# Performance work log

Measured on AMD Instinct MI355X. Metric: run time of the kernel, lower is better.

Reference implementation:

```python
import jax, jax.numpy as jnp
import numpy as np

B, S, A, MSG, C = 524288, 64, 16, 32, 4
CH = 9 + S  # children_states feature dim = 73
EPS = 1e-12  # F.normalize clamp_min eps


def _l2norm(v):
    n = jnp.sqrt(jnp.sum(v * v, axis=-1, keepdims=True))
    return v / jnp.maximum(n, EPS)


def setup_inputs() -> dict:
    key = jax.random.key(0)
    ks = jax.random.split(key, 12)
    def lin(kw, kb, out_d, in_d):
        bound = 1.0 / np.sqrt(in_d)
        W = jax.random.uniform(kw, (out_d, in_d), minval=-bound, maxval=bound, dtype=jnp.float32)
        b = jax.random.uniform(kb, (out_d,), minval=-bound, maxval=bound, dtype=jnp.float32)
        return W, b
    W1, b1 = lin(ks[0], ks[1], 64, S + A)
    W2, b2 = lin(ks[2], ks[3], 64, 64 + MSG)
    W3, b3 = lin(ks[4], ks[5], MSG, 64)
    Wa, ba = lin(ks[6], ks[7], MSG, CH)
    return {
        "x": jax.random.normal(ks[8], (B, S), dtype=jnp.float32),
        "u": jax.random.normal(ks[9], (B, A), dtype=jnp.float32),
        "children_states": jax.random.normal(ks[10], (B, C, CH), dtype=jnp.float32),
        "m": jax.random.normal(ks[11], (B, C * MSG), dtype=jnp.float32),
        "W1": W1, "b1": b1, "W2": W2, "b2": b2, "W3": W3, "b3": b3,
        "Wa": Wa, "ba": ba,
    }


def reference(x, u, children_states, m, W1, b1, W2, b2, W3, b3, Wa, ba):
    # fc1 on cat(x, u), then L2 normalize
    xu = jnp.concatenate([x, u], axis=-1) @ W1.T + b1          # [B, 64]
    xu = _l2norm(xu)
    # attention over children (softmax along child axis, dim=-2)
    att = jax.nn.softmax(children_states @ Wa.T + ba, axis=-2)  # [B, C, MSG]
    mm = m.reshape(*children_states.shape[:-1], -1)             # [B, C, MSG]
    magg = jnp.sum(mm * att, axis=-2)                           # [B, MSG]
    # fused MLP tail
    xum = jnp.tanh(jnp.concatenate([xu, magg], axis=-1))        # [B, 64+MSG]
    xum = jnp.tanh(xum @ W2.T + b2)                             # [B, 64]
    xum = xum @ W3.T + b3                                       # [B, MSG]
    return _l2norm(xum)
```

## Files before the change

### kernel.cpp

```cpp
#include <hip/hip_runtime.h>
#include <cstddef>

typedef __fp16 f16x8 __attribute__((ext_vector_type(8)));
typedef float f32x4 __attribute__((ext_vector_type(4)));
typedef unsigned int uint32;
typedef unsigned short ushort;

constexpr int S = 64, MSG = 32, CH = 73;

constexpr int FC1_OFF = 0;
constexpr int ATT_OFF = 12 * 512;
constexpr int FC2_OFF = 18 * 512;
constexpr int FC3_OFF = 30 * 512;
constexpr int WS_ELEMS = 34 * 512;

__global__ void prep_pack(const float* __restrict__ W1, const float* __restrict__ b1,
                          const float* __restrict__ Wa, const float* __restrict__ ba,
                          const float* __restrict__ W2, const float* __restrict__ W3,
                          ushort* __restrict__ wsf) {
  int idx = blockIdx.x * 256 + threadIdx.x;
  if (idx >= WS_ELEMS) return;
  int tile = idx >> 9;
  int lane = (idx >> 3) & 63;
  int e = idx & 7;
  int jloc = lane & 15;
  int kloc = ((lane >> 4) << 3) + e;
  float v = 0.f;
  if (tile < 12) {
    int t = tile >> 2, f = tile & 3;
    int j = f * 16 + jloc, k = t * 32 + kloc;
    v = (k < 80) ? W1[j * 80 + k] : (k == 80 ? b1[j] : 0.f);
  } else if (tile < 18) {
    int q = tile - 12, t = q >> 1, f = q & 1;
    int j = f * 16 + jloc, k = t * 32 + kloc;
    v = (k < 73) ? Wa[j * 73 + k] : (k == 73 ? ba[j] : 0.f);
  } else if (tile < 30) {
    int q = tile - 18, t = q >> 2, f = q & 3;
    int j = f * 16 + jloc, k = t * 32 + kloc;
    v = W2[j * 96 + k];
  } else {
    int q = tile - 30, t = q >> 1, f = q & 1;
    int j = f * 16 + jloc, k = t * 32 + kloc;
    v = W3[j * 64 + k];
  }
  union { __fp16 h; ushort s; } cv;
  cv.h = (__fp16)v;
  wsf[idx] = cv.s;
}

__device__ __forceinline__ f32x4 mf(f16x8 a, f16x8 b, f32x4 c) {
  return __builtin_amdgcn_mfma_f32_16x16x32_f16(a, b, c, 0, 0, 0);
}
__device__ __forceinline__ uint32 pku(float a, float b) {
  auto r = __builtin_amdgcn_cvt_pkrtz(a, b);
  union { decltype(r) f; uint32 u; } v; v.f = r; return v.u;
}
__device__ __forceinline__ f16x8 packA(const float* f) {
  union { uint32 u[4]; f16x8 h; } r;
  r.u[0] = pku(f[0], f[1]); r.u[1] = pku(f[2], f[3]);
  r.u[2] = pku(f[4], f[5]); r.u[3] = pku(f[6], f[7]);
  return r.h;
}
__device__ __forceinline__ f16x8 packA2(float4 a, float4 b) {
  union { uint32 u[4]; f16x8 h; } r;
  r.u[0] = pku(a.x, a.y); r.u[1] = pku(a.z, a.w);
  r.u[2] = pku(b.x, b.y); r.u[3] = pku(b.z, b.w);
  return r.h;
}
__device__ __forceinline__ float fast_tanh(float v) {
  v = fminf(15.f, fmaxf(-15.f, v));
  float t = __expf(2.f * v);
  return (t - 1.f) * __builtin_amdgcn_rcpf(t + 1.f);
}

constexpr int HT_LD = 104;
constexpr int H2_LD = 72;
constexpr int HBUF_B = 3328;
constexpr int UNION_OFF = 13312;
constexpr int UNION_B = 4672;
constexpr int SMEM_B = 32000;

__launch_bounds__(256)
__global__ void critic_mfma_kernel(
    const float* __restrict__ x, const float* __restrict__ u,
    const float* __restrict__ cs, const float* __restrict__ m,
    const float* __restrict__ b2, const float* __restrict__ b3,
    const ushort* __restrict__ wsf, float* __restrict__ out, int n) {
  __shared__ __attribute__((aligned(16))) unsigned char smem[SMEM_B];

  const int wave = threadIdx.x >> 6;
  const int lane = threadIdx.x & 63;
  const int lm = lane & 15;
  const int lq = lane >> 4;
  const int r0 = (blockIdx.x * 4 + wave) * 16;
  if (r0 >= n) return;

  __fp16* __restrict__ ht = reinterpret_cast<__fp16*>(smem + wave * HBUF_B);
  float* __restrict__ csw = reinterpret_cast<float*>(smem + UNION_OFF + wave * UNION_B);
  __fp16* __restrict__ h2t = reinterpret_cast<__fp16*>(smem + UNION_OFF + wave * UNION_B);

  const float4* __restrict__ xrow4 =
      reinterpret_cast<const float4*>(x + (size_t)(r0 + lm) * S);
  float4 xva = xrow4[2 * lq], xvb = xrow4[2 * lq + 1];
  float4 xvc = xrow4[8 + 2 * lq], xvd = xrow4[9 + 2 * lq];
  const int uq = (lq < 2) ? lq : 0;
  const float4* __restrict__ urow4 =
      reinterpret_cast<const float4*>(u + (size_t)(r0 + lm) * 16);
  float4 uva = urow4[2 * uq], uvb = urow4[2 * uq + 1];

  auto ldB = [&](int off_tile) -> f16x8 {
    return *reinterpret_cast<const f16x8*>(wsf + off_tile + lane * 8);
  };

  f16x8 wa[6];
#pragma unroll
  for (int i = 0; i < 6; ++i) wa[i] = ldB(ATT_OFF + i * 512);

  float4 csr0, csr1, csr2, csr3, csr4;
  {
    const float4* __restrict__ src =
        reinterpret_cast<const float4*>(cs + (size_t)(r0 * 4) * CH);
    csr0 = src[lane];       csr1 = src[64 + lane];
    csr2 = src[128 + lane]; csr3 = src[192 + lane];
    if (lane < 36) csr4 = src[256 + lane];
  }

#pragma unroll
  for (int g = 0; g < 4; ++g) {
    {
      float4* __restrict__ dst = reinterpret_cast<float4*>(csw);
      dst[lane] = csr0;       dst[64 + lane] = csr1;
      dst[128 + lane] = csr2; dst[192 + lane] = csr3;
      if (lane < 36) dst[256 + lane] = csr4;
    }
    float mr[8];
    {
      const float* __restrict__ mrow = m + (size_t)(r0 + 4 * g + lq) * 128;
#pragma unroll
      for (int c = 0; c < 4; ++c) {
        mr[c * 2 + 0] = mrow[c * 32 + lm];
        mr[c * 2 + 1] = mrow[c * 32 + lm + 16];
      }
    }
    if (g < 3) {
      const float4* __restrict__ src =
          reinterpret_cast<const float4*>(cs + (size_t)(r0 * 4 + 16 * (g + 1)) * CH);
      csr0 = src[lane];       csr1 = src[64 + lane];
      csr2 = src[128 + lane]; csr3 = src[192 + lane];
      if (lane < 36) csr4 = src[256 + lane];
    }
    const float* __restrict__ crow = csw + lm * CH;
    f32x4 zac[2] = {{0.f, 0.f, 0.f, 0.f}, {0.f, 0.f, 0.f, 0.f}};
#pragma unroll
    for (int t = 0; t < 3; ++t) {
      float f[8];
      const int kbase = t * 32 + lq * 8;
#pragma unroll
      for (int e = 0; e < 8; ++e) {
        int k = kbase + e;
        f[e] = (k < 73) ? crow[k] : (k == 73 ? 1.f : 0.f);
      }
      f16x8 af = packA(f);
      zac[0] = mf(af, wa[t * 2 + 0], zac[0]);
      zac[1] = mf(af, wa[t * 2 + 1], zac[1]);
    }
#pragma unroll
    for (int f = 0; f < 2; ++f) {
      const int j = lm + 16 * f;
      float e0 = __expf(zac[f][0]);
      float e1 = __expf(zac[f][1]);
      float e2 = __expf(zac[f][2]);
      float e3 = __expf(zac[f][3]);
      float den = (e0 + e1) + (e2 + e3);
      float num = fmaf(mr[0 * 2 + f], e0,
                  fmaf(mr[1 * 2 + f], e1,
                  fmaf(mr[2 * 2 + f], e2, mr[3 * 2 + f] * e3)));
      float mg = num * __builtin_amdgcn_rcpf(den);
      ht[(4 * g + lq) * HT_LD + 64 + j] = (__fp16)fast_tanh(mg);
    }
  }

  f32x4 hac[4] = {{0.f,0.f,0.f,0.f},{0.f,0.f,0.f,0.f},{0.f,0.f,0.f,0.f},{0.f,0.f,0.f,0.f}};
  {
    f16x8 a0 = packA2(xva, xvb);
    f16x8 a1 = packA2(xvc, xvd);
#pragma unroll
    for (int fi = 0; fi < 4; ++fi) hac[fi] = mf(a0, ldB(FC1_OFF + fi * 512), hac[fi]);
#pragma unroll
    for (int fi = 0; fi < 4; ++fi) hac[fi] = mf(a1, ldB(FC1_OFF + (4 + fi) * 512), hac[fi]);
    float f[8];
    float uf[8] = {uva.x, uva.y, uva.z, uva.w, uvb.x, uvb.y, uvb.z, uvb.w};
#pragma unroll
    for (int e = 0; e < 8; ++e) {
      int k = 64 + lq * 8 + e;
      f[e] = (k < 80) ? ((lq < 2) ? uf[e] : 0.f) : (k == 80 ? 1.f : 0.f);
    }
    f16x8 a2f = packA(f);
#pragma unroll
    for (int fi = 0; fi < 4; ++fi) hac[fi] = mf(a2f, ldB(FC1_OFF + (8 + fi) * 512), hac[fi]);
  }
  {
    float rn[4];
#pragma unroll
    for (int reg = 0; reg < 4; ++reg) {
      float s = hac[0][reg] * hac[0][reg];
      s = fmaf(hac[1][reg], hac[1][reg], s);
      s = fmaf(hac[2][reg], hac[2][reg], s);
      s = fmaf(hac[3][reg], hac[3][reg], s);
      s += __shfl_xor(s, 1);
      s += __shfl_xor(s, 2);
      s += __shfl_xor(s, 4);
      s += __shfl_xor(s, 8);
      rn[reg] = __builtin_amdgcn_rcpf(fmaxf(sqrtf(s), 1e-12f));
    }
#pragma unroll
    for (int fi = 0; fi < 4; ++fi)
#pragma unroll
      for (int reg = 0; reg < 4; ++reg)
        ht[(4 * lq + reg) * HT_LD + lm + 16 * fi] =
            (__fp16)fast_tanh(hac[fi][reg] * rn[reg]);
  }

  {
    f32x4 ac2[4] = {{0.f,0.f,0.f,0.f},{0.f,0.f,0.f,0.f},{0.f,0.f,0.f,0.f},{0.f,0.f,0.f,0.f}};
    f16x8 a2[3];
#pragma unroll
    for (int t = 0; t < 3; ++t)
      a2[t] = *reinterpret_cast<const f16x8*>(ht + lm * HT_LD + t * 32 + lq * 8);
#pragma unroll
    for (int t = 0; t < 3; ++t)
#pragma unroll
      for (int fi = 0; fi < 4; ++fi)
        ac2[fi] = mf(a2[t], ldB(FC2_OFF + (t * 4 + fi) * 512), ac2[fi]);
#pragma unroll
    for (int fi = 0; fi < 4; ++fi) {
      float bv = b2[lm + 16 * fi];
#pragma unroll
      for (int reg = 0; reg < 4; ++reg)
        h2t[(4 * lq + reg) * H2_LD + lm + 16 * fi] =
            (__fp16)fast_tanh(ac2[fi][reg] + bv);
    }
  }

  {
    f32x4 o[2] = {{0.f,0.f,0.f,0.f},{0.f,0.f,0.f,0.f}};
    f16x8 a3[2];
#pragma unroll
    for (int t = 0; t < 2; ++t)
      a3[t] = *reinterpret_cast<const f16x8*>(h2t + lm * H2_LD + t * 32 + lq * 8);
#pragma unroll
    for (int t = 0; t < 2; ++t)
#pragma unroll
      for (int fi = 0; fi < 2; ++fi)
        o[fi] = mf(a3[t], ldB(FC3_OFF + (t * 2 + fi) * 512), o[fi]);
#pragma unroll
    for (int fi = 0; fi < 2; ++fi) {
      float bv = b3[lm + 16 * fi];
#pragma unroll
      for (int reg = 0; reg < 4; ++reg) o[fi][reg] += bv;
    }
    float rn2[4];
#pragma unroll
    for (int reg = 0; reg < 4; ++reg) {
      float s = fmaf(o[0][reg], o[0][reg], o[1][reg] * o[1][reg]);
      s += __shfl_xor(s, 1);
      s += __shfl_xor(s, 2);
      s += __shfl_xor(s, 4);
      s += __shfl_xor(s, 8);
      rn2[reg] = __builtin_amdgcn_rcpf(fmaxf(sqrtf(s), 1e-12f));
    }
#pragma unroll
    for (int fi = 0; fi < 2; ++fi)
#pragma unroll
      for (int reg = 0; reg < 4; ++reg)
        out[(size_t)(r0 + 4 * lq + reg) * MSG + lm + 16 * fi] =
            o[fi][reg] * rn2[reg];
  }
}

extern "C" void kernel_launch(void* const* d_in, const int* in_sizes, int n_in,
                              void* d_out, int out_size, void* d_ws, size_t ws_size,
                              hipStream_t stream) {
  const float* x  = (const float*)d_in[0];
  const float* u  = (const float*)d_in[1];
  const float* cs = (const float*)d_in[2];
  const float* m  = (const float*)d_in[3];
  const float* W1 = (const float*)d_in[4];
  const float* b1 = (const float*)d_in[5];
  const float* W2 = (const float*)d_in[6];
  const float* b2 = (const float*)d_in[7];
  const float* W3 = (const float*)d_in[8];
  const float* b3 = (const float*)d_in[9];
  const float* Wa = (const float*)d_in[10];
  const float* ba = (const float*)d_in[11];
  float* out = (float*)d_out;
  ushort* wsf = (ushort*)d_ws;

  const int n = in_sizes[0] / S;

  hipLaunchKernelGGL(prep_pack, dim3((WS_ELEMS + 255) / 256), dim3(256), 0, stream,
                     W1, b1, Wa, ba, W2, W3, wsf);

  const int blocks = (n + 63) / 64;
  hipLaunchKernelGGL(critic_mfma_kernel, dim3(blocks), dim3(256), 0, stream,
                     x, u, cs, m, b2, b3, wsf, out, n);
}
```

Baseline: 223.8 us.

## Process two tiles per wave and prefetch next tile's inputs across iterations

```diff
diff --git a/kernel.cpp b/kernel.cpp
--- a/kernel.cpp
+++ b/kernel.cpp
@@ -92,22 +92,16 @@
   const int lane = threadIdx.x & 63;
   const int lm = lane & 15;
   const int lq = lane >> 4;
-  const int r0 = (blockIdx.x * 4 + wave) * 16;
-  if (r0 >= n) return;
+
+  const int tiles = n >> 4;
+  const int wslots = gridDim.x * 4;
+  const int tbase = blockIdx.x * 4 + wave;
+  if (tbase >= tiles) return;
 
   __fp16* __restrict__ ht = reinterpret_cast<__fp16*>(smem + wave * HBUF_B);
   float* __restrict__ csw = reinterpret_cast<float*>(smem + UNION_OFF + wave * UNION_B);
   __fp16* __restrict__ h2t = reinterpret_cast<__fp16*>(smem + UNION_OFF + wave * UNION_B);
 
-  const float4* __restrict__ xrow4 =
-      reinterpret_cast<const float4*>(x + (size_t)(r0 + lm) * S);
-  float4 xva = xrow4[2 * lq], xvb = xrow4[2 * lq + 1];
-  float4 xvc = xrow4[8 + 2 * lq], xvd = xrow4[9 + 2 * lq];
-  const int uq = (lq < 2) ? lq : 0;
-  const float4* __restrict__ urow4 =
-      reinterpret_cast<const float4*>(u + (size_t)(r0 + lm) * 16);
-  float4 uva = urow4[2 * uq], uvb = urow4[2 * uq + 1];
-
   auto ldB = [&](int off_tile) -> f16x8 {
     return *reinterpret_cast<const f16x8*>(wsf + off_tile + lane * 8);
   };
@@ -117,164 +111,184 @@
   for (int i = 0; i < 6; ++i) wa[i] = ldB(ATT_OFF + i * 512);
 
   float4 csr0, csr1, csr2, csr3, csr4;
-  {
+  float4 xva, xvb, xvc, xvd, uva, uvb;
+
+  auto issue_cs = [&](int r0, int g) {
     const float4* __restrict__ src =
-        reinterpret_cast<const float4*>(cs + (size_t)(r0 * 4) * CH);
+        reinterpret_cast<const float4*>(cs + (size_t)(r0 * 4 + 16 * g) * CH);
     csr0 = src[lane];       csr1 = src[64 + lane];
     csr2 = src[128 + lane]; csr3 = src[192 + lane];
     if (lane < 36) csr4 = src[256 + lane];
-  }
-
-#pragma unroll
-  for (int g = 0; g < 4; ++g) {
+  };
+  auto issue_xu = [&](int r0) {
+    const float4* __restrict__ xrow4 =
+        reinterpret_cast<const float4*>(x + (size_t)(r0 + lm) * S);
+    xva = xrow4[2 * lq]; xvb = xrow4[2 * lq + 1];
+    xvc = xrow4[8 + 2 * lq]; xvd = xrow4[9 + 2 * lq];
+    const int uq = (lq < 2) ? lq : 0;
+    const float4* __restrict__ urow4 =
+        reinterpret_cast<const float4*>(u + (size_t)(r0 + lm) * 16);
+    uva = urow4[2 * uq]; uvb = urow4[2 * uq + 1];
+  };
+
+  issue_cs(tbase << 4, 0);
+  issue_xu(tbase << 4);
+
+  for (int t = 0; t < 2; ++t) {
+    const int tile = tbase + t * wslots;
+    if (tile >= tiles) break;
+    const int r0 = tile << 4;
+    const int ntile = tile + wslots;
+    const bool pre_next = (t == 0) && (ntile < tiles);
+
+#pragma unroll
+    for (int g = 0; g < 4; ++g) {
+      {
+        float4* __restrict__ dst = reinterpret_cast<float4*>(csw);
+        dst[lane] = csr0;       dst[64 + lane] = csr1;
+        dst[128 + lane] = csr2; dst[192 + lane] = csr3;
+        if (lane < 36) dst[256 + lane] = csr4;
+      }
+      float mr[8];
+      {
+        const float* __restrict__ mrow = m + (size_t)(r0 + 4 * g + lq) * 128;
+#pragma unroll
+        for (int c = 0; c < 4; ++c) {
+          mr[c * 2 + 0] = mrow[c * 32 + lm];
+          mr[c * 2 + 1] = mrow[c * 32 + lm + 16];
+        }
+      }
+      if (g < 3) issue_cs(r0, g + 1);
+      else if (pre_next) issue_cs(ntile << 4, 0);
+
+      const float* __restrict__ crow = csw + lm * CH;
+      f32x4 zac[2] = {{0.f, 0.f, 0.f, 0.f}, {0.f, 0.f, 0.f, 0.f}};
+#pragma unroll
+      for (int tt = 0; tt < 3; ++tt) {
+        float f[8];
+        const int kbase = tt * 32 + lq * 8;
+#pragma unroll
+        for (int e = 0; e < 8; ++e) {
+          int k = kbase + e;
+          f[e] = (k < 73) ? crow[k] : (k == 73 ? 1.f : 0.f);
+        }
+        f16x8 af = packA(f);
+        zac[0] = mf(af, wa[tt * 2 + 0], zac[0]);
+        zac[1] = mf(af, wa[tt * 2 + 1], zac[1]);
+      }
+#pragma unroll
+      for (int f = 0; f < 2; ++f) {
+        const int j = lm + 16 * f;
+        float e0 = __expf(zac[f][0]);
+        float e1 = __expf(zac[f][1]);
+        float e2 = __expf(zac[f][2]);
+        float e3 = __expf(zac[f][3]);
+        float den = (e0 + e1) + (e2 + e3);
+        float num = fmaf(mr[0 * 2 + f], e0,
+                    fmaf(mr[1 * 2 + f], e1,
+                    fmaf(mr[2 * 2 + f], e2, mr[3 * 2 + f] * e3)));
+        float mg = num * __builtin_amdgcn_rcpf(den);
+        ht[(4 * g + lq) * HT_LD + 64 + j] = (__fp16)fast_tanh(mg);
+      }
+    }
+
+    f32x4 hac[4] = {{0.f,0.f,0.f,0.f},{0.f,0.f,0.f,0.f},{0.f,0.f,0.f,0.f},{0.f,0.f,0.f,0.f}};
     {
-      float4* __restrict__ dst = reinterpret_cast<float4*>(csw);
-      dst[lane] = csr0;       dst[64 + lane] = csr1;
-      dst[128 + lane] = csr2; dst[192 + lane] = csr3;
-      if (lane < 36) dst[256 + lane] = csr4;
-    }
-    float mr[8];
+      f16x8 a0 = packA2(xva, xvb);
+      f16x8 a1 = packA2(xvc, xvd);
+      float f[8];
+      float uf[8] = {uva.x, uva.y, uva.z, uva.w, uvb.x, uvb.y, uvb.z, uvb.w};
+#pragma unroll
+      for (int e = 0; e < 8; ++e) {
+        int k = 64 + lq * 8 + e;
+        f[e] = (k < 80) ? ((lq < 2) ? uf[e] : 0.f) : (k == 80 ? 1.f : 0.f);
+      }
+      f16x8 a2f = packA(f);
+      if (pre_next) issue_xu(ntile << 4);
+#pragma unroll
+      for (int fi = 0; fi < 4; ++fi) hac[fi] = mf(a0, ldB(FC1_OFF + fi * 512), hac[fi]);
+#pragma unroll
+      for (int fi = 0; fi < 4; ++fi) hac[fi] = mf(a1, ldB(FC1_OFF + (4 + fi) * 512), hac[fi]);
+#pragma unroll
+      for (int fi = 0; fi < 4; ++fi) hac[fi] = mf(a2f, ldB(FC1_OFF + (8 + fi) * 512), hac[fi]);
+    }
     {
-      const float* __restrict__ mrow = m + (size_t)(r0 + 4 * g + lq) * 128;
-#pragma unroll
-      for (int c = 0; c < 4; ++c) {
-        mr[c * 2 + 0] = mrow[c * 32 + lm];
-        mr[c * 2 + 1] = mrow[c * 32 + lm + 16];
-      }
-    }
-    if (g < 3) {
-      const float4* __restrict__ src =
-          reinterpret_cast<const float4*>(cs + (size_t)(r0 * 4 + 16 * (g + 1)) * CH);
-      csr0 = src[lane];       csr1 = src[64 + lane];
-      csr2 = src[128 + lane]; csr3 = src[192 + lane];
-      if (lane < 36) csr4 = src[256 + lane];
-    }
-    const float* __restrict__ crow = csw + lm * CH;
-    f32x4 zac[2] = {{0.f, 0.f, 0.f, 0.f}, {0.f, 0.f, 0.f, 0.f}};
-#pragma unroll
-    for (int t = 0; t < 3; ++t) {
-      float f[8];
-      const int kbase = t * 32 + lq * 8;
-#pragma unroll
-      for (int e = 0; e < 8; ++e) {
-        int k = kbase + e;
-        f[e] = (k < 73) ? crow[k] : (k == 73 ? 1.f : 0.f);
-      }
-      f16x8 af = packA(f);
-      zac[0] = mf(af, wa[t * 2 + 0], zac[0]);
-      zac[1] = mf(af, wa[t * 2 + 1], zac[1]);
-    }
-#pragma unroll
-    for (int f = 0; f < 2; ++f) {
-      const int j = lm + 16 * f;
-      float e0 = __expf(zac[f][0]);
-      float e1 = __expf(zac[f][1]);
-      float e2 = __expf(zac[f][2]);
-      float e3 = __expf(zac[f][3]);
-      float den = (e0 + e1) + (e2 + e3);
-      float num = fmaf(mr[0 * 2 + f], e0,
-                  fmaf(mr[1 * 2 + f], e1,
-                  fmaf(mr[2 * 2 + f], e2, mr[3 * 2 + f] * e3)));
-      float mg = num * __builtin_amdgcn_rcpf(den);
-      ht[(4 * g + lq) * HT_LD + 64 + j] = (__fp16)fast_tanh(mg);
-    }
-  }
-
-  f32x4 hac[4] = {{0.f,0.f,0.f,0.f},{0.f,0.f,0.f,0.f},{0.f,0.f,0.f,0.f},{0.f,0.f,0.f,0.f}};
-  {
-    f16x8 a0 = packA2(xva, xvb);
-    f16x8 a1 = packA2(xvc, xvd);
-#pragma unroll
-    for (int fi = 0; fi < 4; ++fi) hac[fi] = mf(a0, ldB(FC1_OFF + fi * 512), hac[fi]);
-#pragma unroll
-    for (int fi = 0; fi < 4; ++fi) hac[fi] = mf(a1, ldB(FC1_OFF + (4 + fi) * 512), hac[fi]);
-    float f[8];
-    float uf[8] = {uva.x, uva.y, uva.z, uva.w, uvb.x, uvb.y, uvb.z, uvb.w};
-#pragma unroll
-    for (int e = 0; e < 8; ++e) {
-      int k = 64 + lq * 8 + e;
-      f[e] = (k < 80) ? ((lq < 2) ? uf[e] : 0.f) : (k == 80 ? 1.f : 0.f);
-    }
-    f16x8 a2f = packA(f);
-#pragma unroll
-    for (int fi = 0; fi < 4; ++fi) hac[fi] = mf(a2f, ldB(FC1_OFF + (8 + fi) * 512), hac[fi]);
-  }
-  {
-    float rn[4];
-#pragma unroll
-    for (int reg = 0; reg < 4; ++reg) {
-      float s = hac[0][reg] * hac[0][reg];
-      s = fmaf(hac[1][reg], hac[1][reg], s);
-      s = fmaf(hac[2][reg], hac[2][reg], s);
-      s = fmaf(hac[3][reg], hac[3][reg], s);
-      s += __shfl_xor(s, 1);
-      s += __shfl_xor(s, 2);
-      s += __shfl_xor(s, 4);
-      s += __shfl_xor(s, 8);
-      rn[reg] = __builtin_amdgcn_rcpf(fmaxf(sqrtf(s), 1e-12f));
-    }
-#pragma unroll
-    for (int fi = 0; fi < 4; ++fi)
-#pragma unroll
-      for (int reg = 0; reg < 4; ++reg)
-        ht[(4 * lq + reg) * HT_LD + lm + 16 * fi] =
-            (__fp16)fast_tanh(hac[fi][reg] * rn[reg]);
-  }
-
-  {
-    f32x4 ac2[4] = {{0.f,0.f,0.f,0.f},{0.f,0.f,0.f,0.f},{0.f,0.f,0.f,0.f},{0.f,0.f,0.f,0.f}};
-    f16x8 a2[3];
-#pragma unroll
-    for (int t = 0; t < 3; ++t)
-      a2[t] = *reinterpret_cast<const f16x8*>(ht + lm * HT_LD + t * 32 + lq * 8);
-#pragma unroll
-    for (int t = 0; t < 3; ++t)
+      float rn[4];
+#pragma unroll
+      for (int reg = 0; reg < 4; ++reg) {
+        float s = hac[0][reg] * hac[0][reg];
+        s = fmaf(hac[1][reg], hac[1][reg], s);
+        s = fmaf(hac[2][reg], hac[2][reg], s);
+        s = fmaf(hac[3][reg], hac[3][reg], s);
+        s += __shfl_xor(s, 1);
+        s += __shfl_xor(s, 2);
+        s += __shfl_xor(s, 4);
+        s += __shfl_xor(s, 8);
+        rn[reg] = __builtin_amdgcn_rcpf(fmaxf(sqrtf(s), 1e-12f));
+      }
 #pragma unroll
       for (int fi = 0; fi < 4; ++fi)
-        ac2[fi] = mf(a2[t], ldB(FC2_OFF + (t * 4 + fi) * 512), ac2[fi]);
-#pragma unroll
-    for (int fi = 0; fi < 4; ++fi) {
-      float bv = b2[lm + 16 * fi];
-#pragma unroll
-      for (int reg = 0; reg < 4; ++reg)
-        h2t[(4 * lq + reg) * H2_LD + lm + 16 * fi] =
-            (__fp16)fast_tanh(ac2[fi][reg] + bv);
-    }
-  }
-
-  {
-    f32x4 o[2] = {{0.f,0.f,0.f,0.f},{0.f,0.f,0.f,0.f}};
-    f16x8 a3[2];
-#pragma unroll
-    for (int t = 0; t < 2; ++t)
-      a3[t] = *reinterpret_cast<const f16x8*>(h2t + lm * H2_LD + t * 32 + lq * 8);
-#pragma unroll
-    for (int t = 0; t < 2; ++t)
+#pragma unroll
+        for (int reg = 0; reg < 4; ++reg)
+          ht[(4 * lq + reg) * HT_LD + lm + 16 * fi] =
+              (__fp16)fast_tanh(hac[fi][reg] * rn[reg]);
+    }
+
+    {
+      f32x4 ac2[4] = {{0.f,0.f,0.f,0.f},{0.f,0.f,0.f,0.f},{0.f,0.f,0.f,0.f},{0.f,0.f,0.f,0.f}};
+      f16x8 a2[3];
+#pragma unroll
+      for (int tt = 0; tt < 3; ++tt)
+        a2[tt] = *reinterpret_cast<const f16x8*>(ht + lm * HT_LD + tt * 32 + lq * 8);
+#pragma unroll
+      for (int tt = 0; tt < 3; ++tt)
+#pragma unroll
+        for (int fi = 0; fi < 4; ++fi)
+          ac2[fi] = mf(a2[tt], ldB(FC2_OFF + (tt * 4 + fi) * 512), ac2[fi]);
+#pragma unroll
+      for (int fi = 0; fi < 4; ++fi) {
+        float bv = b2[lm + 16 * fi];
+#pragma unroll
+        for (int reg = 0; reg < 4; ++reg)
+          h2t[(4 * lq + reg) * H2_LD + lm + 16 * fi] =
+              (__fp16)fast_tanh(ac2[fi][reg] + bv);
+      }
+    }
+
+    {
+      f32x4 o[2] = {{0.f,0.f,0.f,0.f},{0.f,0.f,0.f,0.f}};
+      f16x8 a3[2];
+#pragma unroll
+      for (int tt = 0; tt < 2; ++tt)
+        a3[tt] = *reinterpret_cast<const f16x8*>(h2t + lm * H2_LD + tt * 32 + lq * 8);
+#pragma unroll
+      for (int tt = 0; tt < 2; ++tt)
+#pragma unroll
+        for (int fi = 0; fi < 2; ++fi)
+          o[fi] = mf(a3[tt], ldB(FC3_OFF + (tt * 2 + fi) * 512), o[fi]);
+#pragma unroll
+      for (int fi = 0; fi < 2; ++fi) {
+        float bv = b3[lm + 16 * fi];
+#pragma unroll
+        for (int reg = 0; reg < 4; ++reg) o[fi][reg] += bv;
+      }
+      float rn2[4];
+#pragma unroll
+      for (int reg = 0; reg < 4; ++reg) {
+        float s = fmaf(o[0][reg], o[0][reg], o[1][reg] * o[1][reg]);
+        s += __shfl_xor(s, 1);
+        s += __shfl_xor(s, 2);
+        s += __shfl_xor(s, 4);
+        s += __shfl_xor(s, 8);
+        rn2[reg] = __builtin_amdgcn_rcpf(fmaxf(sqrtf(s), 1e-12f));
+      }
 #pragma unroll
       for (int fi = 0; fi < 2; ++fi)
-        o[fi] = mf(a3[t], ldB(FC3_OFF + (t * 2 + fi) * 512), o[fi]);
-#pragma unroll
-    for (int fi = 0; fi < 2; ++fi) {
-      float bv = b3[lm + 16 * fi];
-#pragma unroll
-      for (int reg = 0; reg < 4; ++reg) o[fi][reg] += bv;
-    }
-    float rn2[4];
-#pragma unroll
-    for (int reg = 0; reg < 4; ++reg) {
-      float s = fmaf(o[0][reg], o[0][reg], o[1][reg] * o[1][reg]);
-      s += __shfl_xor(s, 1);
-      s += __shfl_xor(s, 2);
-      s += __shfl_xor(s, 4);
-      s += __shfl_xor(s, 8);
-      rn2[reg] = __builtin_amdgcn_rcpf(fmaxf(sqrtf(s), 1e-12f));
-    }
-#pragma unroll
-    for (int fi = 0; fi < 2; ++fi)
-#pragma unroll
-      for (int reg = 0; reg < 4; ++reg)
-        out[(size_t)(r0 + 4 * lq + reg) * MSG + lm + 16 * fi] =
-            o[fi][reg] * rn2[reg];
+#pragma unroll
+        for (int reg = 0; reg < 4; ++reg)
+          out[(size_t)(r0 + 4 * lq + reg) * MSG + lm + 16 * fi] =
+              o[fi][reg] * rn2[reg];
+    }
   }
 }
 
@@ -297,11 +311,12 @@
   ushort* wsf = (ushort*)d_ws;
 
   const int n = in_sizes[0] / S;
+  const int tiles = (n + 15) / 16;
 
   hipLaunchKernelGGL(prep_pack, dim3((WS_ELEMS + 255) / 256), dim3(256), 0, stream,
                      W1, b1, Wa, ba, W2, W3, wsf);
 
-  const int blocks = (n + 63) / 64;
+  const int blocks = (tiles + 7) / 8;
   hipLaunchKernelGGL(critic_mfma_kernel, dim3(blocks), dim3(256), 0, stream,
                      x, u, cs, m, b2, b3, wsf, out, n);
 }
```

Measured after the change: 230.8 us. 1.03x slower.
